# Optimization experiments

Hardware: AMD Instinct MI355X
Metric: run time of the kernel (lower is better)

The kernel has to match this reference:

```python
import jax, jax.numpy as jnp
import numpy as np


def setup_inputs() -> dict:
    key = jax.random.key(0)
    k1, k2 = jax.random.split(key)
    # NCHW input activations
    x = jax.random.normal(k1, (32, 256, 56, 56), dtype=jnp.float32)
    # OIHW weight; centered small-uniform so sign() is +/-1 with equal probability
    # (torch init is rand()*0.001, all-positive, which would make sign degenerate
    #  for kernel testing; magnitude scale kept comparable)
    weight = (jax.random.uniform(k2, (256, 256, 3, 3), dtype=jnp.float32) - 0.5) * 0.002
    return {"x": x, "weight": weight}


def reference(x, weight):
    # per-output-channel scaling factor: mean |w| over (in, kh, kw), detached
    scale = jax.lax.stop_gradient(
        jnp.mean(jnp.abs(weight), axis=(1, 2, 3), keepdims=True)
    )  # [O,1,1,1]
    w_clip = jnp.clip(weight, -1.0, 1.0)
    # STE: forward value = scale * sign(w); gradient flows through clip(w)
    binary_w = jax.lax.stop_gradient(scale * jnp.sign(weight) - w_clip) + w_clip
    y = jax.lax.conv_general_dilated(
        x,
        binary_w,
        window_strides=(1, 1),
        padding=((1, 1), (1, 1)),
        dimension_numbers=("NCHW", "OIHW", "NCHW"),
        feature_group_count=1,
    )
    return y
```

## Files before the change

### kernel.cpp

```cpp
#include <hip/hip_runtime.h>
#include <stdint.h>

typedef __attribute__((ext_vector_type(8))) short bf16x8;
typedef __attribute__((ext_vector_type(4))) float f32x4;
typedef __attribute__((ext_vector_type(8))) unsigned short u16x8;

#define N_IMG 32
#define CI 256
#define CO 256
#define HH_ 56
#define WW_ 56
#define HP 58
#define WP 58
#define SPP (HP*WP)
#define SPI (HH_*WW_)

#define XB_BYTES ((size_t)N_IMG*SPP*CI*2)
#define W2_OFF   XB_BYTES
#define W2_BYTES ((size_t)9*CO*CI*2)
#define SCALE_OFF (W2_OFF + W2_BYTES)

#define KCP 40

__global__ __launch_bounds__(256) void zero_xb_k(uint4* __restrict__ p) {
  p[(size_t)blockIdx.x*256 + threadIdx.x] = make_uint4(0u,0u,0u,0u);
}

__global__ __launch_bounds__(256) void nchw2nhwc_k(const float* __restrict__ x,
                                                   unsigned short* __restrict__ xb) {
  __shared__ float tile[64*33];
  int b = blockIdx.x;
  int n = b / 392; int r = b - n*392;
  int cc = r / 49; int t0 = (r - cc*49) * 64;
  int t = threadIdx.x;
  int sp = t & 63; int ci4 = t >> 6;
  const float* src = x + ((size_t)(n*CI + cc*32))*SPI + t0;
#pragma unroll
  for (int i = 0; i < 8; ++i) {
    int c = i*4 + ci4;
    tile[sp*33 + c] = src[(size_t)c*SPI + sp];
  }
  __syncthreads();
  int osp = t >> 2; int cg = t & 3;
  int spg = t0 + osp;
  int h = spg / 56; int w = spg - h*56;
  int psp = (h+1)*58 + (w+1);
  unsigned int pk[4];
#pragma unroll
  for (int j = 0; j < 4; ++j) {
    unsigned int u0 = __builtin_bit_cast(unsigned int, tile[osp*33 + cg*8 + j*2]);
    unsigned int u1 = __builtin_bit_cast(unsigned int, tile[osp*33 + cg*8 + j*2 + 1]);
    u0 = (u0 + 0x7fffu + ((u0 >> 16) & 1u)) >> 16;
    u1 = (u1 + 0x7fffu + ((u1 >> 16) & 1u)) >> 16;
    pk[j] = u0 | (u1 << 16);
  }
  uint4 v; v.x = pk[0]; v.y = pk[1]; v.z = pk[2]; v.w = pk[3];
  *(uint4*)(&xb[((size_t)n*SPP + psp)*CI + cc*32 + cg*8]) = v;
}

__global__ __launch_bounds__(256) void prep_w_k(const float* __restrict__ wt,
                                                unsigned short* __restrict__ w2,
                                                float* __restrict__ scale) {
  int o = blockIdx.x; int t = threadIdx.x;
  float s = 0.f;
#pragma unroll
  for (int k = t, it = 0; it < 9; ++it, k += 256) {
    float v = wt[(size_t)o*2304 + k];
    s += fabsf(v);
    int c = k / 9; int tap = k - c*9;
    unsigned short sg = (v > 0.f) ? (unsigned short)0x3F80u
                       : ((v < 0.f) ? (unsigned short)0xBF80u : (unsigned short)0u);
    w2[((size_t)tap*CO + o)*CI + c] = sg;
  }
  __shared__ float red[4];
#pragma unroll
  for (int off = 32; off > 0; off >>= 1) s += __shfl_down(s, off, 64);
  if ((t & 63) == 0) red[t >> 6] = s;
  __syncthreads();
  if (t == 0) scale[o] = (red[0]+red[1]+red[2]+red[3]) * (1.0f/2304.0f);
}

__global__ __launch_bounds__(256, 2) void binconv_k(
    const unsigned short* __restrict__ xb,
    const unsigned short* __restrict__ w2,
    const float* __restrict__ scale,
    float* __restrict__ out) {
  __shared__ unsigned short s_patch[300*KCP];
  __shared__ unsigned short s_w[576*KCP];

  int bid = blockIdx.x;
  int ot = bid & 3; int pt = bid >> 2;
  int n = pt / 14; int rem = pt - n*14;
  int ht = rem >> 1; int wt = rem & 1;
  int h0 = ht*8, w0 = wt*28, ob = ot*64;
  int tid = threadIdx.x;
  int lane = tid & 63, wid = tid >> 6;
  int wo = wid >> 1, wp = wid & 1;
  int lrow = lane & 15, lgrp = lane >> 4;

  int pb[7];
#pragma unroll
  for (int f = 0; f < 7; ++f) {
    int p = wp*112 + f*16 + lrow;
    int th = p / 28; int tw = p - th*28;
    pb[f] = (th*30 + tw)*KCP + lgrp*8;
  }
  int ab0 = (wo*32 + lrow)*KCP + lgrp*8;

  f32x4 acc[2][7];
#pragma unroll
  for (int m = 0; m < 2; ++m)
#pragma unroll
    for (int f = 0; f < 7; ++f) {
      f32x4 z = {0.f, 0.f, 0.f, 0.f};
      acc[m][f] = z;
    }

  const size_t xbase = ((size_t)n*SPP + (size_t)h0*WP + w0)*CI;

  for (int cc = 0; cc < 8; ++cc) {
    __syncthreads();
#pragma unroll
    for (int u = tid, it = 0; it < 5; ++it, u += 256) {
      if (u < 1200) {
        int rr = u >> 2, cg = u & 3;
        int hh = rr / 30, ww2 = rr - hh*30;
        *(u16x8*)&s_patch[rr*KCP + cg*8] =
          *(const u16x8*)&xb[xbase + ((size_t)hh*WP + ww2)*CI + (size_t)cc*32 + cg*8];
      }
    }
#pragma unroll
    for (int u = tid, it = 0; it < 9; ++it, u += 256) {
      int tap = u >> 8, r2 = u & 255, oo = r2 >> 2, cg = r2 & 3;
      *(u16x8*)&s_w[(tap*64 + oo)*KCP + cg*8] =
        *(const u16x8*)&w2[((size_t)tap*CO + ob + oo)*CI + (size_t)cc*32 + cg*8];
    }
    __syncthreads();
#pragma unroll
    for (int tap = 0; tap < 9; ++tap) {
      const int dh = tap / 3, dw = tap - dh*3;
      const int toff = (dh*30 + dw)*KCP;
      const int woff = tap*64*KCP;
      bf16x8 a0 = *(const bf16x8*)&s_w[woff + ab0];
      bf16x8 a1 = *(const bf16x8*)&s_w[woff + ab0 + 16*KCP];
      bf16x8 bv[7];
#pragma unroll
      for (int f = 0; f < 7; ++f)
        bv[f] = *(const bf16x8*)&s_patch[pb[f] + toff];
#pragma unroll
      for (int f = 0; f < 7; ++f) {
        acc[0][f] = __builtin_amdgcn_mfma_f32_16x16x32_bf16(a0, bv[f], acc[0][f], 0, 0, 0);
        acc[1][f] = __builtin_amdgcn_mfma_f32_16x16x32_bf16(a1, bv[f], acc[1][f], 0, 0, 0);
      }
    }
  }

  float sc[2][4];
#pragma unroll
  for (int m = 0; m < 2; ++m)
#pragma unroll
    for (int r = 0; r < 4; ++r)
      sc[m][r] = scale[ob + wo*32 + m*16 + lgrp*4 + r];

#pragma unroll
  for (int f = 0; f < 7; ++f) {
    int p = wp*112 + f*16 + lrow;
    int th = p / 28; int tw = p - th*28;
    size_t spo = (size_t)(h0+th)*WW_ + (w0+tw);
#pragma unroll
    for (int m = 0; m < 2; ++m) {
      int o = ob + wo*32 + m*16 + lgrp*4;
      float* dst = out + ((size_t)n*CO + o)*SPI + spo;
#pragma unroll
      for (int r = 0; r < 4; ++r)
        dst[(size_t)r*SPI] = acc[m][f][r] * sc[m][r];
    }
  }
}

extern "C" void kernel_launch(void* const* d_in, const int* in_sizes, int n_in,
                              void* d_out, int out_size, void* d_ws, size_t ws_size,
                              hipStream_t stream) {
  const float* x  = (const float*)d_in[0];
  const float* wt = (const float*)d_in[1];
  float* out = (float*)d_out;
  unsigned short* xb = (unsigned short*)d_ws;
  unsigned short* w2 = (unsigned short*)((char*)d_ws + W2_OFF);
  float* scale = (float*)((char*)d_ws + SCALE_OFF);

  zero_xb_k<<<13456, 256, 0, stream>>>((uint4*)d_ws);
  nchw2nhwc_k<<<12544, 256, 0, stream>>>(x, xb);
  prep_w_k<<<256, 256, 0, stream>>>(wt, w2, scale);
  binconv_k<<<1792, 256, 0, stream>>>(xb, w2, scale, out);
}
```

Baseline: 343.1 us.

## Rework conv pipeline: double-buffered LDS DMA, global weight loads, larger tiles, border-only zeroing

```diff
diff --git a/kernel.cpp b/kernel.cpp
--- a/kernel.cpp
+++ b/kernel.cpp
@@ -3,7 +3,6 @@
 
 typedef __attribute__((ext_vector_type(8))) short bf16x8;
 typedef __attribute__((ext_vector_type(4))) float f32x4;
-typedef __attribute__((ext_vector_type(8))) unsigned short u16x8;
 
 #define N_IMG 32
 #define CI 256
@@ -20,57 +19,87 @@
 #define W2_BYTES ((size_t)9*CO*CI*2)
 #define SCALE_OFF (W2_OFF + W2_BYTES)
 
-#define KCP 40
-
-__global__ __launch_bounds__(256) void zero_xb_k(uint4* __restrict__ p) {
-  p[(size_t)blockIdx.x*256 + threadIdx.x] = make_uint4(0u,0u,0u,0u);
+__device__ __forceinline__ unsigned int pack_bf16(float a, float b) {
+  unsigned int u0 = __builtin_bit_cast(unsigned int, a);
+  unsigned int u1 = __builtin_bit_cast(unsigned int, b);
+  u0 = (u0 + 0x7fffu + ((u0 >> 16) & 1u)) >> 16;
+  u1 = (u1 + 0x7fffu + ((u1 >> 16) & 1u)) >> 16;
+  return u0 | (u1 << 16);
+}
+
+__device__ __forceinline__ void gl_lds16(const void* g, void* l) {
+  __builtin_amdgcn_global_load_lds(
+      (const __attribute__((address_space(1))) unsigned int*)g,
+      (__attribute__((address_space(3))) unsigned int*)l, 16, 0, 0);
+}
+
+__global__ __launch_bounds__(256) void border_zero_k(unsigned short* __restrict__ xb) {
+  int gid = blockIdx.x*256 + threadIdx.x;
+  int cell = gid >> 5, part = gid & 31;
+  int n = cell / 228, b = cell - n*228;
+  int h, w;
+  if (b < 58)       { h = 0;          w = b;        }
+  else if (b < 116) { h = 57;         w = b - 58;   }
+  else if (b < 172) { h = b - 116 + 1; w = 0;       }
+  else              { h = b - 172 + 1; w = 57;      }
+  uint4 z = make_uint4(0u,0u,0u,0u);
+  *(uint4*)&xb[((size_t)n*SPP + (size_t)h*WP + w)*CI + part*8] = z;
 }
 
 __global__ __launch_bounds__(256) void nchw2nhwc_k(const float* __restrict__ x,
                                                    unsigned short* __restrict__ xb) {
-  __shared__ float tile[64*33];
-  int b = blockIdx.x;
-  int n = b / 392; int r = b - n*392;
-  int cc = r / 49; int t0 = (r - cc*49) * 64;
+  __shared__ float tile[64*64];
+  int bid = blockIdx.x;
+  int n = bid / 196; int r = bid - n*196;
+  int cb = r / 49;   int t0 = (r - cb*49) * 64;
   int t = threadIdx.x;
-  int sp = t & 63; int ci4 = t >> 6;
-  const float* src = x + ((size_t)(n*CI + cc*32))*SPI + t0;
-#pragma unroll
-  for (int i = 0; i < 8; ++i) {
-    int c = i*4 + ci4;
-    tile[sp*33 + c] = src[(size_t)c*SPI + sp];
+  int row = t >> 4, l16 = t & 15;
+  const float* src = x + ((size_t)(n*CI + cb*64))*SPI + t0;
+#pragma unroll
+  for (int it = 0; it < 4; ++it) {
+    int c = it*16 + row;
+    float4 v = *(const float4*)&src[(size_t)c*SPI + l16*4];
+    const float* vf = (const float*)&v;
+#pragma unroll
+    for (int j = 0; j < 4; ++j) {
+      int sp = l16*4 + j;
+      int cs = c ^ (((sp >> 2) & 7) << 3);
+      tile[sp*64 + cs] = vf[j];
+    }
   }
   __syncthreads();
-  int osp = t >> 2; int cg = t & 3;
-  int spg = t0 + osp;
-  int h = spg / 56; int w = spg - h*56;
-  int psp = (h+1)*58 + (w+1);
-  unsigned int pk[4];
-#pragma unroll
-  for (int j = 0; j < 4; ++j) {
-    unsigned int u0 = __builtin_bit_cast(unsigned int, tile[osp*33 + cg*8 + j*2]);
-    unsigned int u1 = __builtin_bit_cast(unsigned int, tile[osp*33 + cg*8 + j*2 + 1]);
-    u0 = (u0 + 0x7fffu + ((u0 >> 16) & 1u)) >> 16;
-    u1 = (u1 + 0x7fffu + ((u1 >> 16) & 1u)) >> 16;
-    pk[j] = u0 | (u1 << 16);
-  }
-  uint4 v; v.x = pk[0]; v.y = pk[1]; v.z = pk[2]; v.w = pk[3];
-  *(uint4*)(&xb[((size_t)n*SPP + psp)*CI + cc*32 + cg*8]) = v;
+#pragma unroll
+  for (int it = 0; it < 2; ++it) {
+    int u = it*256 + t;
+    int sp = u >> 3, part = u & 7;
+    int g = (part*8) ^ (((sp >> 2) & 7) << 3);
+    float4 f0 = *(const float4*)&tile[sp*64 + g];
+    float4 f1 = *(const float4*)&tile[sp*64 + g + 4];
+    const float* a0 = (const float*)&f0; const float* a1 = (const float*)&f1;
+    uint4 pk;
+    pk.x = pack_bf16(a0[0], a0[1]);
+    pk.y = pack_bf16(a0[2], a0[3]);
+    pk.z = pack_bf16(a1[0], a1[1]);
+    pk.w = pack_bf16(a1[2], a1[3]);
+    int spg = t0 + sp; int h = spg / 56; int w = spg - h*56;
+    size_t psp = (size_t)(h+1)*WP + (w+1);
+    *(uint4*)&xb[((size_t)n*SPP + psp)*CI + cb*64 + part*8] = pk;
+  }
 }
 
 __global__ __launch_bounds__(256) void prep_w_k(const float* __restrict__ wt,
                                                 unsigned short* __restrict__ w2,
                                                 float* __restrict__ scale) {
   int o = blockIdx.x; int t = threadIdx.x;
+  const float* wr = wt + (size_t)o*2304 + t*9;
   float s = 0.f;
 #pragma unroll
-  for (int k = t, it = 0; it < 9; ++it, k += 256) {
-    float v = wt[(size_t)o*2304 + k];
+  for (int tap = 0; tap < 9; ++tap) {
+    float v = wr[tap];
     s += fabsf(v);
-    int c = k / 9; int tap = k - c*9;
     unsigned short sg = (v > 0.f) ? (unsigned short)0x3F80u
                        : ((v < 0.f) ? (unsigned short)0xBF80u : (unsigned short)0u);
-    w2[((size_t)tap*CO + o)*CI + c] = sg;
+    w2[((size_t)tap*CO + o)*CI + t] = sg;
   }
   __shared__ float red[4];
 #pragma unroll
@@ -80,19 +109,20 @@
   if (t == 0) scale[o] = (red[0]+red[1]+red[2]+red[3]) * (1.0f/2304.0f);
 }
 
+#define PCH 1280
 __global__ __launch_bounds__(256, 2) void binconv_k(
     const unsigned short* __restrict__ xb,
     const unsigned short* __restrict__ w2,
     const float* __restrict__ scale,
     float* __restrict__ out) {
-  __shared__ unsigned short s_patch[300*KCP];
-  __shared__ unsigned short s_w[576*KCP];
+  __shared__ unsigned short sp_buf[2][PCH*8];
 
   int bid = blockIdx.x;
-  int ot = bid & 3; int pt = bid >> 2;
-  int n = pt / 14; int rem = pt - n*14;
-  int ht = rem >> 1; int wt = rem & 1;
-  int h0 = ht*8, w0 = wt*28, ob = ot*64;
+  int orig = (bid & 7)*112 + (bid >> 3);
+  int ot = orig & 1, pt = orig >> 1;
+  int n = pt / 14, rem = pt - n*14;
+  int ht = rem >> 1, wtl = rem & 1;
+  int h0 = ht*8, w0 = wtl*28, OB = ot*128;
   int tid = threadIdx.x;
   int lane = tid & 63, wid = tid >> 6;
   int wo = wid >> 1, wp = wid & 1;
@@ -103,64 +133,75 @@
   for (int f = 0; f < 7; ++f) {
     int p = wp*112 + f*16 + lrow;
     int th = p / 28; int tw = p - th*28;
-    pb[f] = (th*30 + tw)*KCP + lgrp*8;
-  }
-  int ab0 = (wo*32 + lrow)*KCP + lgrp*8;
-
-  f32x4 acc[2][7];
-#pragma unroll
-  for (int m = 0; m < 2; ++m)
+    pb[f] = (th*30 + tw)*32 + lgrp*8;
+  }
+
+  const unsigned short* wA = w2 + (((size_t)(OB + wo*64 + lrow)) << 8) + lgrp*8;
+
+  const unsigned short* xsrc = xb + ((size_t)n*SPP + (size_t)h0*WP + w0)*CI;
+
+  f32x4 acc[4][7];
+#pragma unroll
+  for (int m = 0; m < 4; ++m)
 #pragma unroll
     for (int f = 0; f < 7; ++f) {
       f32x4 z = {0.f, 0.f, 0.f, 0.f};
       acc[m][f] = z;
     }
 
-  const size_t xbase = ((size_t)n*SPP + (size_t)h0*WP + w0)*CI;
+#define STAGE(BUF, CC)                                                        \
+  {                                                                           \
+    const unsigned short* g_ = xsrc + (CC)*32;                                \
+    _Pragma("unroll")                                                         \
+    for (int rdi = 0; rdi < 5; ++rdi) {                                       \
+      int u = rdi*256 + tid;                                                  \
+      if (u < 1200) {                                                         \
+        int rr = u >> 2, cg = u & 3;                                          \
+        int hh = rr / 30, ww = rr - hh*30;                                    \
+        gl_lds16(g_ + ((size_t)hh*WP + ww)*CI + cg*8,                         \
+                 &sp_buf[BUF][(size_t)(rdi*256 + (tid & ~63))*8]);            \
+      }                                                                       \
+    }                                                                         \
+  }
+
+  STAGE(0, 0);
+  __syncthreads();
 
   for (int cc = 0; cc < 8; ++cc) {
-    __syncthreads();
-#pragma unroll
-    for (int u = tid, it = 0; it < 5; ++it, u += 256) {
-      if (u < 1200) {
-        int rr = u >> 2, cg = u & 3;
-        int hh = rr / 30, ww2 = rr - hh*30;
-        *(u16x8*)&s_patch[rr*KCP + cg*8] =
-          *(const u16x8*)&xb[xbase + ((size_t)hh*WP + ww2)*CI + (size_t)cc*32 + cg*8];
-      }
-    }
-#pragma unroll
-    for (int u = tid, it = 0; it < 9; ++it, u += 256) {
-      int tap = u >> 8, r2 = u & 255, oo = r2 >> 2, cg = r2 & 3;
-      *(u16x8*)&s_w[(tap*64 + oo)*KCP + cg*8] =
-        *(const u16x8*)&w2[((size_t)tap*CO + ob + oo)*CI + (size_t)cc*32 + cg*8];
-    }
-    __syncthreads();
+    int cur = cc & 1;
+    if (cc < 7) STAGE(cur ^ 1, cc + 1);
+
+    const unsigned short* aCC = wA + cc*32;
 #pragma unroll
     for (int tap = 0; tap < 9; ++tap) {
       const int dh = tap / 3, dw = tap - dh*3;
-      const int toff = (dh*30 + dw)*KCP;
-      const int woff = tap*64*KCP;
-      bf16x8 a0 = *(const bf16x8*)&s_w[woff + ab0];
-      bf16x8 a1 = *(const bf16x8*)&s_w[woff + ab0 + 16*KCP];
+      const int toff = (dh*30 + dw)*32;
+      const unsigned short* aP = aCC + ((size_t)tap << 16);
+      bf16x8 a0 = *(const bf16x8*)(aP);
+      bf16x8 a1 = *(const bf16x8*)(aP + 4096);
+      bf16x8 a2 = *(const bf16x8*)(aP + 8192);
+      bf16x8 a3 = *(const bf16x8*)(aP + 12288);
       bf16x8 bv[7];
 #pragma unroll
       for (int f = 0; f < 7; ++f)
-        bv[f] = *(const bf16x8*)&s_patch[pb[f] + toff];
+        bv[f] = *(const bf16x8*)&sp_buf[cur][pb[f] + toff];
 #pragma unroll
       for (int f = 0; f < 7; ++f) {
         acc[0][f] = __builtin_amdgcn_mfma_f32_16x16x32_bf16(a0, bv[f], acc[0][f], 0, 0, 0);
         acc[1][f] = __builtin_amdgcn_mfma_f32_16x16x32_bf16(a1, bv[f], acc[1][f], 0, 0, 0);
+        acc[2][f] = __builtin_amdgcn_mfma_f32_16x16x32_bf16(a2, bv[f], acc[2][f], 0, 0, 0);
+        acc[3][f] = __builtin_amdgcn_mfma_f32_16x16x32_bf16(a3, bv[f], acc[3][f], 0, 0, 0);
       }
     }
-  }
-
-  float sc[2][4];
-#pragma unroll
-  for (int m = 0; m < 2; ++m)
+    __syncthreads();
+  }
+
+  float sc[4][4];
+#pragma unroll
+  for (int m = 0; m < 4; ++m)
 #pragma unroll
     for (int r = 0; r < 4; ++r)
-      sc[m][r] = scale[ob + wo*32 + m*16 + lgrp*4 + r];
+      sc[m][r] = scale[OB + wo*64 + m*16 + lgrp*4 + r];
 
 #pragma unroll
   for (int f = 0; f < 7; ++f) {
@@ -168,8 +209,8 @@
     int th = p / 28; int tw = p - th*28;
     size_t spo = (size_t)(h0+th)*WW_ + (w0+tw);
 #pragma unroll
-    for (int m = 0; m < 2; ++m) {
-      int o = ob + wo*32 + m*16 + lgrp*4;
+    for (int m = 0; m < 4; ++m) {
+      int o = OB + wo*64 + m*16 + lgrp*4;
       float* dst = out + ((size_t)n*CO + o)*SPI + spo;
 #pragma unroll
       for (int r = 0; r < 4; ++r)
@@ -188,8 +229,8 @@
   unsigned short* w2 = (unsigned short*)((char*)d_ws + W2_OFF);
   float* scale = (float*)((char*)d_ws + SCALE_OFF);
 
-  zero_xb_k<<<13456, 256, 0, stream>>>((uint4*)d_ws);
-  nchw2nhwc_k<<<12544, 256, 0, stream>>>(x, xb);
+  border_zero_k<<<912, 256, 0, stream>>>(xb);
+  nchw2nhwc_k<<<6272, 256, 0, stream>>>(x, xb);
   prep_w_k<<<256, 256, 0, stream>>>(wt, w2, scale);
-  binconv_k<<<1792, 256, 0, stream>>>(xb, w2, scale, out);
-}
+  binconv_k<<<896, 256, 0, stream>>>(xb, w2, scale, out);
+}
```

New measurement: 346.3 us. About the same (+0.9%).
